# Kernel optimization log

Measured on AMD Instinct MI355X. Metric: run time of the kernel, lower is better.

The kernel has to match this reference:

```python
import jax, jax.numpy as jnp
import numpy as np

B, L, D, H, NW = 1, 4096, 1024, 16, 8
W = L // NW   # window size = 512
HD = D // H   # head dim = 64


def _mha(x, w_in, b_in, w_out, b_out):
    # torch.nn.MultiheadAttention self-attention: x [b, s, D]
    b, s, d = x.shape
    qkv = x @ w_in.T + b_in                      # [b, s, 3D]
    q, k, v = jnp.split(qkv, 3, axis=-1)
    q = q.reshape(b, s, H, HD).transpose(0, 2, 1, 3) * (HD ** -0.5)
    k = k.reshape(b, s, H, HD).transpose(0, 2, 1, 3)
    v = v.reshape(b, s, H, HD).transpose(0, 2, 1, 3)
    attn = jax.nn.softmax(jnp.einsum('bhqd,bhkd->bhqk', q, k), axis=-1)
    o = jnp.einsum('bhqk,bhkd->bhqd', attn, v)   # [b, H, s, HD]
    o = o.transpose(0, 2, 1, 3).reshape(b, s, d)
    return o @ w_out.T + b_out


def setup_inputs() -> dict:
    key = jax.random.key(0)
    ks = jax.random.split(key, 10)
    sc = 0.02  # keep attention logits in a sane range
    return {
        'x': jax.random.normal(ks[0], (B, L, D), jnp.float32),
        'rotary_factor': jax.random.uniform(ks[1], (1, D), jnp.float32, 0.0, 0.1),
        'win_w_in': jax.random.normal(ks[2], (NW, 3 * D, D), jnp.float32) * sc,
        'win_b_in': jax.random.normal(ks[3], (NW, 3 * D), jnp.float32) * sc,
        'win_w_out': jax.random.normal(ks[4], (NW, D, D), jnp.float32) * sc,
        'win_b_out': jax.random.normal(ks[5], (NW, D), jnp.float32) * sc,
        'fin_w_in': jax.random.normal(ks[6], (3 * D, D), jnp.float32) * sc,
        'fin_b_in': jax.random.normal(ks[7], (3 * D,), jnp.float32) * sc,
        'fin_w_out': jax.random.normal(ks[8], (D, D), jnp.float32) * sc,
        'fin_b_out': jax.random.normal(ks[9], (D,), jnp.float32) * sc,
    }


def reference(x, rotary_factor, win_w_in, win_b_in, win_w_out, win_b_out,
              fin_w_in, fin_b_in, fin_w_out, fin_b_out):
    # rotary-style additive embedding: angles [L, D/2] -> cat(cos, sin) [L, D]
    pos = jnp.arange(L, dtype=jnp.float32)[:, None]
    inv = 10000.0 ** (jnp.arange(0, D, 2, dtype=jnp.float32) / D)  # [D/2]
    ang = rotary_factor[:, :D // 2] * pos / inv                     # [L, D/2]
    x = x + jnp.concatenate([jnp.cos(ang), jnp.sin(ang)], axis=-1)  # [B, L, D]

    # per-window self-attention with per-window weights, residual add
    xw = x.reshape(B, NW, W, D)
    wout = jax.vmap(_mha, in_axes=(1, 0, 0, 0, 0), out_axes=1)(
        xw, win_w_in, win_b_in, win_w_out, win_b_out)
    x = (xw + wout).reshape(B, L, D)

    # final global self-attention
    return _mha(x, fin_w_in, fin_b_in, fin_w_out, fin_b_out)
```

## Files before the change

### kernel.cpp

```cpp
#include <hip/hip_runtime.h>
#include <hip/hip_bf16.h>

#define L_ 4096
#define D_ 1024
#define H_ 16
#define HD_ 64
#define NW_ 8
#define WIN_ 512
#define TD (3*D_)

typedef __attribute__((ext_vector_type(8))) short bf16x8;
typedef __attribute__((ext_vector_type(4))) float f32x4;

typedef __attribute__((address_space(1))) const void GVp;
typedef __attribute__((address_space(3))) void LVp;

__device__ __forceinline__ f32x4 mfma16(bf16x8 a, bf16x8 b, f32x4 c) {
    return __builtin_amdgcn_mfma_f32_16x16x32_bf16(a, b, c, 0, 0, 0);
}

__device__ __forceinline__ short f2bfs(float f) {
    __hip_bfloat16 h = __float2bfloat16(f);
    return *reinterpret_cast<short*>(&h);
}

__device__ __forceinline__ float lclamp(float v, float c) {
    return fminf(fmaxf(v, -c), c);
}

__device__ __forceinline__ float rot_add(const float* rf, int l, int d) {
    const int j = d & 511;
    const float r = rf[j];
    const float inv = exp2f((float)j * 0.02595256324130752f);
    const float ang = r * (float)l / inv;
    return (d < 512) ? cosf(ang) : sinf(ang);
}

__global__ __launch_bounds__(256) void rotary_k(
    const float* __restrict__ x,
    const float* __restrict__ rf,
    __hip_bfloat16* __restrict__ x1b)
{
    const int idx = blockIdx.x * 256 + threadIdx.x;
    const int l = idx >> 10;
    const int d = idx & 1023;
    const float v = x[idx] + rot_add(rf, l, d);
    x1b[idx] = __float2bfloat16(lclamp(v, 1.0e4f));
}

__global__ __launch_bounds__(256) void wcvt_all(
    const float* __restrict__ w0, const float* __restrict__ w1,
    const float* __restrict__ w2, const float* __restrict__ w3,
    __hip_bfloat16* __restrict__ o0, __hip_bfloat16* __restrict__ o1,
    __hip_bfloat16* __restrict__ o2, __hip_bfloat16* __restrict__ o3)
{
    const unsigned i = (blockIdx.x * 256u + threadIdx.x) * 4u;
    const float* s; __hip_bfloat16* d; unsigned j;
    if (i < 25165824u)      { s = w0; d = o0; j = i; }
    else if (i < 33554432u) { s = w1; d = o1; j = i - 25165824u; }
    else if (i < 36700160u) { s = w2; d = o2; j = i - 33554432u; }
    else                    { s = w3; d = o3; j = i - 36700160u; }
    float4 v = *(const float4*)&s[j];
    short t[4] = {f2bfs(v.x), f2bfs(v.y), f2bfs(v.z), f2bfs(v.w)};
    *(uint2*)&d[j] = *(uint2*)t;
}

template<int WF32>
__global__ __launch_bounds__(256) void gemm_u(
    const __hip_bfloat16* __restrict__ A,
    const void* __restrict__ Wv,
    const float* __restrict__ bias,
    const float* __restrict__ xin,
    const float* __restrict__ rf,
    int residMode,
    __hip_bfloat16* __restrict__ Cb,
    float* __restrict__ Cf,
    int N, int wStrideW, int wStrideB)
{
    int bn = blockIdx.x, bm = blockIdx.y;
    {
        const int gx = gridDim.x, gy = gridDim.y;
        const int nblk = gx * gy;
        if ((nblk & 7) == 0) {
            const int lid = blockIdx.y * gx + blockIdx.x;
            const int per = nblk >> 3;
            const int t = (lid & 7) * per + (lid >> 3);
            bn = t / gy;
            bm = t - bn * gy;
        }
    }
    const int m0 = bm * 128;
    const int n0 = bn * 128;
    const int win = m0 / WIN_;

    const short* Wb = (const short*)Wv + (WF32 ? 0 : (size_t)win * (size_t)wStrideW);
    const float* Wf = (const float*)Wv + (WF32 ? (size_t)win * (size_t)wStrideW : 0);
    const float* Bp = bias + (size_t)win * (size_t)wStrideB;

    __shared__ __align__(16) short As[2][128 * 32];
    __shared__ __align__(16) short Bs[2][WF32 ? 128 * 64 : 128 * 32];

    const int tid  = threadIdx.x;
    const int lane = tid & 63;
    const int wave = tid >> 6;
    const int wm = (wave & 1) * 64;
    const int wn = (wave >> 1) * 64;
    const int lrow = lane & 15;
    const int kg   = lane >> 4;

    const int sA0 = tid,        rA0 = sA0 >> 2, gA0 = (sA0 & 3) ^ ((rA0 >> 1) & 3);
    const int sA1 = tid + 256,  rA1 = sA1 >> 2, gA1 = (sA1 & 3) ^ ((rA1 >> 1) & 3);
    const short* Asrc0 = (const short*)A + (size_t)(m0 + rA0) * D_ + gA0 * 8;
    const short* Asrc1 = (const short*)A + (size_t)(m0 + rA1) * D_ + gA1 * 8;

    const short* Wsrc0 = Wb + (size_t)(n0 + rA0) * D_ + gA0 * 8;
    const short* Wsrc1 = Wb + (size_t)(n0 + rA1) * D_ + gA1 * 8;

    const float* Fsrc[4];
    if (WF32) {
        #pragma unroll
        for (int j = 0; j < 4; j++) {
            const int s = tid + 256 * j;
            const int row = s >> 3;
            const int g8 = (s & 7) ^ (row & 7);
            Fsrc[j] = Wf + (size_t)(n0 + row) * D_ + g8 * 4;
        }
    }

    auto stage = [&](int k0, int buf) {
        __builtin_amdgcn_global_load_lds((GVp*)(Asrc0 + k0), (LVp*)&As[buf][wave * 512],        16, 0, 0);
        __builtin_amdgcn_global_load_lds((GVp*)(Asrc1 + k0), (LVp*)&As[buf][2048 + wave * 512], 16, 0, 0);
        if (WF32) {
            #pragma unroll
            for (int j = 0; j < 4; j++)
                __builtin_amdgcn_global_load_lds((GVp*)(Fsrc[j] + k0), (LVp*)&Bs[buf][j * 2048 + wave * 512], 16, 0, 0);
        } else {
            __builtin_amdgcn_global_load_lds((GVp*)(Wsrc0 + k0), (LVp*)&Bs[buf][wave * 512],        16, 0, 0);
            __builtin_amdgcn_global_load_lds((GVp*)(Wsrc1 + k0), (LVp*)&Bs[buf][2048 + wave * 512], 16, 0, 0);
        }
    };

    const f32x4 zero4 = {0.f, 0.f, 0.f, 0.f};
    f32x4 acc[4][4];
    #pragma unroll
    for (int i = 0; i < 4; i++)
        #pragma unroll
        for (int jj = 0; jj < 4; jj++) acc[i][jj] = zero4;

    stage(0, 0);
    const int nsteps = D_ / 32;
    for (int i = 0; i < nsteps; i++) {
        const int cur = i & 1;
        __syncthreads();
        if (i + 1 < nsteps) stage((i + 1) * 32, 1 - cur);

        bf16x8 af[4], bfr[4];
        #pragma unroll
        for (int ii = 0; ii < 4; ii++) {
            const int ar_ = wm + ii * 16 + lrow;
            af[ii] = *(const bf16x8*)&As[cur][ar_ * 32 + ((kg ^ ((ar_ >> 1) & 3)) * 8)];
        }
        #pragma unroll
        for (int jj = 0; jj < 4; jj++) {
            const int wr_ = wn + jj * 16 + lrow;
            if (WF32) {
                const float4 wlo = *(const float4*)&Bs[cur][wr_ * 64 + (((2 * kg)     ^ (wr_ & 7)) * 8)];
                const float4 whi = *(const float4*)&Bs[cur][wr_ * 64 + (((2 * kg + 1) ^ (wr_ & 7)) * 8)];
                short t[8] = {f2bfs(wlo.x), f2bfs(wlo.y), f2bfs(wlo.z), f2bfs(wlo.w),
                              f2bfs(whi.x), f2bfs(whi.y), f2bfs(whi.z), f2bfs(whi.w)};
                bfr[jj] = *(const bf16x8*)t;
            } else {
                bfr[jj] = *(const bf16x8*)&Bs[cur][wr_ * 32 + ((kg ^ ((wr_ >> 1) & 3)) * 8)];
            }
        }
        #pragma unroll
        for (int ii = 0; ii < 4; ii++)
            #pragma unroll
            for (int jj = 0; jj < 4; jj++)
                acc[ii][jj] = mfma16(af[ii], bfr[jj], acc[ii][jj]);
    }

    #pragma unroll
    for (int jj = 0; jj < 4; jj++) {
        const int col = n0 + wn + jj * 16 + lrow;
        const float bv = Bp[col];
        #pragma unroll
        for (int i = 0; i < 4; i++) {
            #pragma unroll
            for (int r = 0; r < 4; r++) {
                const int row = m0 + wm + i * 16 + kg * 4 + r;
                float v = acc[i][jj][r] + bv;
                if (residMode) {
                    v += xin[(size_t)row * D_ + col] + rot_add(rf, row, col);
                }
                v = lclamp(v, 1.0e4f);
                if (Cf) Cf[(size_t)row * N + col] = v;
                else    Cb[(size_t)row * N + col] = __float2bfloat16(v);
            }
        }
    }
}

__global__ __launch_bounds__(256) void transpose_v(
    const __hip_bfloat16* __restrict__ qkv,
    __hip_bfloat16* __restrict__ Vt)
{
    __shared__ __align__(16) short Ts[64 * 72];
    const int t = threadIdx.x;
    const int l0 = blockIdx.x * 64;
    const int h = blockIdx.y;
    #pragma unroll
    for (int p = 0; p < 2; p++) {
        const int idx = p * 256 + t;
        const int key = idx >> 3, part = idx & 7;
        *(uint4*)&Ts[key * 72 + part * 8] =
            *(const uint4*)&qkv[(size_t)(l0 + key) * TD + 2 * D_ + h * HD_ + part * 8];
    }
    __syncthreads();
    #pragma unroll
    for (int p = 0; p < 2; p++) {
        const int idx = p * 256 + t;
        const int vd = idx >> 3, part = idx & 7;
        short tmp[8];
        #pragma unroll
        for (int j = 0; j < 8; j++) tmp[j] = Ts[(part * 8 + j) * 72 + vd];
        *(uint4*)&Vt[(size_t)(h * HD_ + vd) * L_ + l0 + part * 8] = *(uint4*)tmp;
    }
}

__global__ __launch_bounds__(256, 3) void attn_k(
    const __hip_bfloat16* __restrict__ qkv,
    const __hip_bfloat16* __restrict__ Vt,
    __hip_bfloat16* __restrict__ o,
    int Sw)
{
    const int tid  = threadIdx.x;
    const int lane = tid & 63;
    const int wave = tid >> 6;
    const int lrow = lane & 15;
    const int kg   = lane >> 4;

    int bx = blockIdx.x, by = blockIdx.y, bz = blockIdx.z;
    {
        const int gx = gridDim.x, gy = gridDim.y, gz = gridDim.z;
        const int nblk = gx * gy * gz;
        if ((nblk & 7) == 0) {
            const int lid = (blockIdx.z * gy + blockIdx.y) * gx + blockIdx.x;
            const int per = nblk >> 3;
            const int t = (lid & 7) * per + (lid >> 3);
            bx = t % gx;
            const int rest = t / gx;
            by = rest % gy;
            bz = rest / gy;
        }
    }
    const int h = by;
    const int wbase = bz * Sw;
    const int q0 = wbase + bx * 64 + wave * 16;

    const short* Kglb = reinterpret_cast<const short*>(qkv)
                        + (size_t)wbase * TD + D_ + h * HD_;
    const short* Vtglb = reinterpret_cast<const short*>(Vt)
                         + (size_t)h * HD_ * L_ + wbase;
    const __hip_bfloat16* Q = qkv + (size_t)q0 * TD + h * HD_;

    __shared__ __align__(16) short Ks[2][64 * 64];
    __shared__ __align__(16) short Vs[2][64 * 64];
    __shared__ __align__(16) short Ps[4][16 * 72];
    short* myP = &Ps[wave][0];

    const bf16x8 qf0 = *(const bf16x8*)&Q[(size_t)lrow * TD + kg * 8];
    const bf16x8 qf1 = *(const bf16x8*)&Q[(size_t)lrow * TD + 32 + kg * 8];

    const f32x4 zero4 = {0.f, 0.f, 0.f, 0.f};
    float lacc[4];
    f32x4 oacc[4];
    #pragma unroll
    for (int r = 0; r < 4; r++) lacc[r] = 0.f;
    #pragma unroll
    for (int t = 0; t < 4; t++) oacc[t] = zero4;

    auto stage = [&](int c, int buf) {
        const int s0 = (wave & 1) * 256;
        if (wave < 2) {
            #pragma unroll
            for (int j = 0; j < 4; j++) {
                const int s = s0 + j * 64 + lane;
                const int r = s >> 3;
                const int cb = (s & 7) ^ (r & 7);
                const short* src = Kglb + (size_t)(c + r) * TD + cb * 8;
                __builtin_amdgcn_global_load_lds(
                    (GVp*)src, (LVp*)&Ks[buf][(s0 + j * 64) * 8], 16, 0, 0);
            }
        } else {
            #pragma unroll
            for (int j = 0; j < 4; j++) {
                const int s = s0 + j * 64 + lane;
                const int r = s >> 3;
                const int cb = (s & 7) ^ (r & 7);
                const short* src = Vtglb + (size_t)r * L_ + c + cb * 8;
                __builtin_amdgcn_global_load_lds(
                    (GVp*)src, (LVp*)&Vs[buf][(s0 + j * 64) * 8], 16, 0, 0);
            }
        }
    };

    const int ntiles = Sw >> 6;
    stage(0, 0);

    const float SC = 0.18033688011112042f;
    const float MB = -23.083120654223414f;

    for (int i = 0; i < ntiles; i++) {
        const int cur = i & 1;
        __syncthreads();
        if (i + 1 < ntiles) stage((i + 1) << 6, 1 - cur);

        const short* Kl = Ks[cur];
        const short* Vl = Vs[cur];
        const int sw = lrow & 7;

        f32x4 s[4];
        #pragma unroll
        for (int kt = 0; kt < 4; kt++) {
            const int key = kt * 16 + lrow;
            bf16x8 k0 = *(const bf16x8*)&Kl[key * 64 + ((kg     ^ sw) * 8)];
            bf16x8 k1 = *(const bf16x8*)&Kl[key * 64 + (((kg+4) ^ sw) * 8)];
            f32x4 acc = zero4;
            acc = mfma16(qf0, k0, acc);
            acc = mfma16(qf1, k1, acc);
            s[kt] = acc;
        }

        asm volatile("" ::: "memory");
        #pragma unroll
        for (int kt = 0; kt < 4; kt++) {
            #pragma unroll
            for (int r = 0; r < 4; r++) {
                const float p = exp2f(fmaf(s[kt][r], SC, MB));
                lacc[r] += p;
                myP[(kg * 4 + r) * 72 + kt * 16 + lrow] = f2bfs(p);
            }
        }
        asm volatile("s_waitcnt lgkmcnt(0)" ::: "memory");
        const bf16x8 pf0 = *(const bf16x8*)&myP[lrow * 72 + kg * 8];
        const bf16x8 pf1 = *(const bf16x8*)&myP[lrow * 72 + 32 + kg * 8];

        #pragma unroll
        for (int t = 0; t < 4; t++) {
            const int vd = t * 16 + lrow;
            bf16x8 v0 = *(const bf16x8*)&Vl[vd * 64 + ((kg     ^ sw) * 8)];
            bf16x8 v1 = *(const bf16x8*)&Vl[vd * 64 + (((kg+4) ^ sw) * 8)];
            oacc[t] = mfma16(pf0, v0, oacc[t]);
            oacc[t] = mfma16(pf1, v1, oacc[t]);
        }
    }

    #pragma unroll
    for (int off = 1; off < 16; off <<= 1)
        #pragma unroll
        for (int r = 0; r < 4; r++)
            lacc[r] += __shfl_xor(lacc[r], off, 64);

    #pragma unroll
    for (int t = 0; t < 4; t++) {
        #pragma unroll
        for (int r = 0; r < 4; r++) {
            const int row = q0 + kg * 4 + r;
            const int col = h * HD_ + t * 16 + lrow;
            o[(size_t)row * D_ + col] =
                __float2bfloat16(lclamp(oacc[t][r] / lacc[r], 1.0e4f));
        }
    }
}

extern "C" void kernel_launch(void* const* d_in, const int* in_sizes, int n_in,
                              void* d_out, int out_size, void* d_ws, size_t ws_size,
                              hipStream_t stream)
{
    const float* x   = (const float*)d_in[0];
    const float* rf  = (const float*)d_in[1];
    const float* wwi = (const float*)d_in[2];
    const float* wbi = (const float*)d_in[3];
    const float* wwo = (const float*)d_in[4];
    const float* wbo = (const float*)d_in[5];
    const float* fwi = (const float*)d_in[6];
    const float* fbi = (const float*)d_in[7];
    const float* fwo = (const float*)d_in[8];
    const float* fbo = (const float*)d_in[9];

    char* ws = (char*)d_ws;
    __hip_bfloat16* qkv = (__hip_bfloat16*)(ws);
    __hip_bfloat16* ob  = (__hip_bfloat16*)(ws + (24u << 20));
    __hip_bfloat16* xsc = (__hip_bfloat16*)d_out;
    __hip_bfloat16* Vt  = (__hip_bfloat16*)d_out;

    const size_t MB1 = 1u << 20;
    const int bw = (ws_size >= 104 * MB1) ? 1 : 0;

    __hip_bfloat16* wwib = (__hip_bfloat16*)(ws + 32 * MB1);
    __hip_bfloat16* wwob = (__hip_bfloat16*)(ws + 80 * MB1);
    __hip_bfloat16* fwib = (__hip_bfloat16*)(ws + 96 * MB1);
    __hip_bfloat16* fwob = (__hip_bfloat16*)(ws + 102 * MB1);
    if (bw) {
        wcvt_all<<<dim3(36864), 256, 0, stream>>>(
            wwi, wwo, fwi, fwo, wwib, wwob, fwib, fwob);
    }

    rotary_k<<<dim3(L_ * D_ / 256), 256, 0, stream>>>(x, rf, xsc);

    if (bw) gemm_u<0><<<dim3(TD / 128, L_ / 128), 256, 0, stream>>>(
        xsc, wwib, wbi, nullptr, nullptr, 0, qkv, nullptr, TD, TD * D_, TD);
    else    gemm_u<1><<<dim3(TD / 128, L_ / 128), 256, 0, stream>>>(
        xsc, wwi,  wbi, nullptr, nullptr, 0, qkv, nullptr, TD, TD * D_, TD);

    transpose_v<<<dim3(L_ / 64, H_), 256, 0, stream>>>(qkv, Vt);

    attn_k<<<dim3(WIN_ / 64, H_, NW_), 256, 0, stream>>>(qkv, Vt, ob, WIN_);

    if (bw) gemm_u<0><<<dim3(D_ / 128, L_ / 128), 256, 0, stream>>>(
        ob, wwob, wbo, x, rf, 1, xsc, nullptr, D_, D_ * D_, D_);
    else    gemm_u<1><<<dim3(D_ / 128, L_ / 128), 256, 0, stream>>>(
        ob, wwo,  wbo, x, rf, 1, xsc, nullptr, D_, D_ * D_, D_);

    if (bw) gemm_u<0><<<dim3(TD / 128, L_ / 128), 256, 0, stream>>>(
        xsc, fwib, fbi, nullptr, nullptr, 0, qkv, nullptr, TD, 0, 0);
    else    gemm_u<1><<<dim3(TD / 128, L_ / 128), 256, 0, stream>>>(
        xsc, fwi,  fbi, nullptr, nullptr, 0, qkv, nullptr, TD, 0, 0);

    transpose_v<<<dim3(L_ / 64, H_), 256, 0, stream>>>(qkv, Vt);

    attn_k<<<dim3(L_ / 64, H_, 1), 256, 0, stream>>>(qkv, Vt, ob, L_);

    if (bw) gemm_u<0><<<dim3(D_ / 128, L_ / 128), 256, 0, stream>>>(
        ob, fwob, fbo, nullptr, nullptr, 0, nullptr, (float*)d_out, D_, 0, 0);
    else    gemm_u<1><<<dim3(D_ / 128, L_ / 128), 256, 0, stream>>>(
        ob, fwo,  fbo, nullptr, nullptr, 0, nullptr, (float*)d_out, D_, 0, 0);
}
```

Before: 669.5 us.

## Add 256x256-tile 8-wave GEMM with 4-stage LDS pipeline for QKV projections

Adds a new bf16 GEMM kernel, gemm8, which uses 256x256 output tiles, 512 threads (8 waves, each computing 128x64), and a 4-buffer LDS ring fed by global_load_lds. A and B loads are interleaved with the two MFMA halves under setprio and explicit vmcnt waits. It replaces the 128x128 gemm_u for both QKV in-projections (window and final) when bf16 weights are available. The larger tile is meant to raise arithmetic intensity and hide memory latency better. In exchange it launches only 192 blocks, which may underfill the GPU, and it uses 128KB of LDS and many accumulator registers.

```diff
diff --git a/kernel.cpp b/kernel.cpp
--- a/kernel.cpp
+++ b/kernel.cpp
@@ -63,6 +63,139 @@
     float4 v = *(const float4*)&s[j];
     short t[4] = {f2bfs(v.x), f2bfs(v.y), f2bfs(v.z), f2bfs(v.w)};
     *(uint2*)&d[j] = *(uint2*)t;
+}
+
+__global__ __launch_bounds__(512) void gemm8(
+    const __hip_bfloat16* __restrict__ A,
+    const __hip_bfloat16* __restrict__ Wb,
+    const float* __restrict__ bias,
+    __hip_bfloat16* __restrict__ Cb,
+    int N, int wStrideW, int wStrideB)
+{
+    int bn = blockIdx.x, bm = blockIdx.y;
+    {
+        const int gx = gridDim.x, gy = gridDim.y;
+        const int nblk = gx * gy;
+        if ((nblk & 7) == 0) {
+            const int lid = blockIdx.y * gx + blockIdx.x;
+            const int per = nblk >> 3;
+            const int t = (lid & 7) * per + (lid >> 3);
+            bn = t / gy;
+            bm = t - bn * gy;
+        }
+    }
+    const int m0 = bm * 256;
+    const int n0 = bn * 256;
+    const int win = m0 / WIN_;
+    const short* Wp = (const short*)Wb + (size_t)win * (size_t)wStrideW;
+    const float* Bp = bias + (size_t)win * (size_t)wStrideB;
+
+    __shared__ __align__(16) short As[4][256 * 32];
+    __shared__ __align__(16) short Bs[4][256 * 32];
+
+    const int tid  = threadIdx.x;
+    const int lane = tid & 63;
+    const int wave = tid >> 6;
+    const int lrow = lane & 15;
+    const int kg   = lane >> 4;
+    const int wrow = (wave >> 2) * 128;
+    const int wcol = (wave & 3) * 64;
+
+    const int sl0 = tid,       r0_ = sl0 >> 2, g0_ = (sl0 & 3) ^ (r0_ & 3);
+    const int sl1 = tid + 512, r1_ = sl1 >> 2, g1_ = (sl1 & 3) ^ (r1_ & 3);
+    const short* Asrc0 = (const short*)A + (size_t)(m0 + r0_) * D_ + g0_ * 8;
+    const short* Asrc1 = (const short*)A + (size_t)(m0 + r1_) * D_ + g1_ * 8;
+    const short* Wsrc0 = Wp + (size_t)(n0 + r0_) * D_ + g0_ * 8;
+    const short* Wsrc1 = Wp + (size_t)(n0 + r1_) * D_ + g1_ * 8;
+
+    auto stageA = [&](int t, int b) {
+        __builtin_amdgcn_global_load_lds((GVp*)(Asrc0 + t * 32), (LVp*)&As[b][wave * 512], 16, 0, 0);
+        __builtin_amdgcn_global_load_lds((GVp*)(Asrc1 + t * 32), (LVp*)&As[b][4096 + wave * 512], 16, 0, 0);
+    };
+    auto stageB = [&](int t, int b) {
+        __builtin_amdgcn_global_load_lds((GVp*)(Wsrc0 + t * 32), (LVp*)&Bs[b][wave * 512], 16, 0, 0);
+        __builtin_amdgcn_global_load_lds((GVp*)(Wsrc1 + t * 32), (LVp*)&Bs[b][4096 + wave * 512], 16, 0, 0);
+    };
+
+    int aoff[8], boff[4];
+    #pragma unroll
+    for (int i = 0; i < 8; i++) {
+        const int row = wrow + i * 16 + lrow;
+        aoff[i] = (row * 4 + (kg ^ (row & 3))) * 8;
+    }
+    #pragma unroll
+    for (int j = 0; j < 4; j++) {
+        const int row = wcol + j * 16 + lrow;
+        boff[j] = (row * 4 + (kg ^ (row & 3))) * 8;
+    }
+
+    const f32x4 zero4 = {0.f, 0.f, 0.f, 0.f};
+    f32x4 acc[8][4];
+    #pragma unroll
+    for (int i = 0; i < 8; i++)
+        #pragma unroll
+        for (int j = 0; j < 4; j++) acc[i][j] = zero4;
+
+    stageA(0, 0); stageB(0, 0);
+    stageA(1, 1); stageB(1, 1);
+    stageA(2, 2); stageB(2, 2);
+    asm volatile("s_waitcnt vmcnt(8)" ::: "memory");
+    __builtin_amdgcn_s_barrier();
+
+    const int NT = D_ / 32;
+    #pragma unroll 1
+    for (int t = 0; t < NT; ++t) {
+        const int cb = t & 3;
+        const short* Ab = As[cb];
+        const short* Bb = Bs[cb];
+        bf16x8 af[4], bfr[4];
+
+        #pragma unroll
+        for (int j = 0; j < 4; j++) bfr[j] = *(const bf16x8*)&Bb[boff[j]];
+        #pragma unroll
+        for (int i = 0; i < 4; i++) af[i] = *(const bf16x8*)&Ab[aoff[i]];
+        if (t + 3 < NT) stageA(t + 3, (t + 3) & 3);
+        __builtin_amdgcn_s_barrier();
+        __builtin_amdgcn_s_setprio(1);
+        #pragma unroll
+        for (int i = 0; i < 4; i++)
+            #pragma unroll
+            for (int j = 0; j < 4; j++)
+                acc[i][j] = mfma16(af[i], bfr[j], acc[i][j]);
+        __builtin_amdgcn_s_setprio(0);
+        __builtin_amdgcn_s_barrier();
+
+        #pragma unroll
+        for (int i = 0; i < 4; i++) af[i] = *(const bf16x8*)&Ab[aoff[4 + i]];
+        if (t + 3 < NT) stageB(t + 3, (t + 3) & 3);
+        if (t <= NT - 4)      asm volatile("s_waitcnt vmcnt(8)" ::: "memory");
+        else if (t == NT - 3) asm volatile("s_waitcnt vmcnt(4)" ::: "memory");
+        else if (t == NT - 2) asm volatile("s_waitcnt vmcnt(0)" ::: "memory");
+        __builtin_amdgcn_s_barrier();
+        __builtin_amdgcn_s_setprio(1);
+        #pragma unroll
+        for (int i = 0; i < 4; i++)
+            #pragma unroll
+            for (int j = 0; j < 4; j++)
+                acc[4 + i][j] = mfma16(af[i], bfr[j], acc[4 + i][j]);
+        __builtin_amdgcn_s_setprio(0);
+        __builtin_amdgcn_s_barrier();
+    }
+
+    #pragma unroll
+    for (int j = 0; j < 4; j++) {
+        const int col = n0 + wcol + j * 16 + lrow;
+        const float bv = Bp[col];
+        #pragma unroll
+        for (int i = 0; i < 8; i++) {
+            #pragma unroll
+            for (int r = 0; r < 4; r++) {
+                const int row = m0 + wrow + i * 16 + kg * 4 + r;
+                const float v = lclamp(acc[i][j][r] + bv, 1.0e4f);
+                Cb[(size_t)row * N + col] = __float2bfloat16(v);
+            }
+        }
+    }
 }
 
 template<int WF32>
@@ -409,8 +542,8 @@
 
     rotary_k<<<dim3(L_ * D_ / 256), 256, 0, stream>>>(x, rf, xsc);
 
-    if (bw) gemm_u<0><<<dim3(TD / 128, L_ / 128), 256, 0, stream>>>(
-        xsc, wwib, wbi, nullptr, nullptr, 0, qkv, nullptr, TD, TD * D_, TD);
+    if (bw) gemm8<<<dim3(TD / 256, L_ / 256), 512, 0, stream>>>(
+        xsc, wwib, wbi, qkv, TD, TD * D_, TD);
     else    gemm_u<1><<<dim3(TD / 128, L_ / 128), 256, 0, stream>>>(
         xsc, wwi,  wbi, nullptr, nullptr, 0, qkv, nullptr, TD, TD * D_, TD);
 
@@ -423,8 +556,8 @@
     else    gemm_u<1><<<dim3(D_ / 128, L_ / 128), 256, 0, stream>>>(
         ob, wwo,  wbo, x, rf, 1, xsc, nullptr, D_, D_ * D_, D_);
 
-    if (bw) gemm_u<0><<<dim3(TD / 128, L_ / 128), 256, 0, stream>>>(
-        xsc, fwib, fbi, nullptr, nullptr, 0, qkv, nullptr, TD, 0, 0);
+    if (bw) gemm8<<<dim3(TD / 256, L_ / 256), 512, 0, stream>>>(
+        xsc, fwib, fbi, qkv, TD, 0, 0);
     else    gemm_u<1><<<dim3(TD / 128, L_ / 128), 256, 0, stream>>>(
         xsc, fwi,  fbi, nullptr, nullptr, 0, qkv, nullptr, TD, 0, 0);
 
```

Measured after the change: 594.4 us. 11.2% less time.
